# Kernel optimization log

Measured on AMD Instinct MI355X. Metric: run time of the kernel, lower is better.

## Reference

```python
import jax, jax.numpy as jnp
import numpy as np

B, S, H, NH = 1, 4096, 1024, 16
HD = H // NH  # 64


def _rope_tables(seq_len, dim):
    inv_freq = 1.0 / (10000.0 ** (np.arange(0, dim, 2, dtype=np.float32) / dim))
    t = np.arange(seq_len, dtype=np.float32)
    freqs = np.outer(t, inv_freq)                 # [S, dim/2]
    emb = np.concatenate([freqs, freqs], axis=-1)  # [S, dim]
    return jnp.asarray(np.cos(emb)), jnp.asarray(np.sin(emb))


def setup_inputs() -> dict:
    key = jax.random.key(0)
    ks = jax.random.split(key, 5)
    hidden_states = jax.random.normal(ks[0], (B, S, H), dtype=jnp.float32)
    scale = 1.0 / np.sqrt(H)
    Wq = jax.random.normal(ks[1], (H, H), dtype=jnp.float32) * scale
    Wk = jax.random.normal(ks[2], (H, H), dtype=jnp.float32) * scale
    Wv = jax.random.normal(ks[3], (H, H), dtype=jnp.float32) * scale
    Wo = jax.random.normal(ks[4], (H, H), dtype=jnp.float32) * scale
    cos, sin = _rope_tables(S, HD)
    # additive causal mask [1,1,S,S]
    causal = jnp.where(
        jnp.tril(jnp.ones((S, S), dtype=bool)), 0.0, jnp.float32(-1e9)
    )[None, None]
    return {
        "hidden_states": hidden_states,
        "cos": cos,
        "sin": sin,
        "attention_mask": causal,
        "Wq": Wq,
        "Wk": Wk,
        "Wv": Wv,
        "Wo": Wo,
    }


def _rotate_half(x):
    x1, x2 = jnp.split(x, 2, axis=-1)
    return jnp.concatenate([-x2, x1], axis=-1)


def _apply_rope(q, k, cos, sin):
    # q,k: [B,NH,S,HD]; cos/sin: [S,HD] -> broadcast [1,1,S,HD]
    cos = cos[None, None]
    sin = sin[None, None]
    q = q * cos + _rotate_half(q) * sin
    k = k * cos + _rotate_half(k) * sin
    return q, k


def reference(hidden_states, cos, sin, attention_mask, Wq, Wk, Wv, Wo):
    bsz, q_len, _ = hidden_states.shape
    q = hidden_states @ Wq.T
    k = hidden_states @ Wk.T
    v = hidden_states @ Wv.T
    # [B,S,H] -> [B,NH,S,HD]
    def split_heads(x):
        return x.reshape(bsz, q_len, NH, HD).transpose(0, 2, 1, 3)
    q, k, v = split_heads(q), split_heads(k), split_heads(v)
    q, k = _apply_rope(q, k, cos, sin)
    scores = jnp.einsum("bhqd,bhkd->bhqk", q, k) / jnp.sqrt(jnp.float32(HD))
    scores = scores + attention_mask
    attn = jax.nn.softmax(scores, axis=-1)
    out = jnp.einsum("bhqk,bhkd->bhqd", attn, v)
    out = out.transpose(0, 2, 1, 3).reshape(bsz, q_len, H)
    return out @ Wo.T
```

## Files before the change

### kernel.cpp

```cpp
#include <hip/hip_runtime.h>

#define S_LEN 4096
#define NHEADS 16
#define HD 64
#define HDIM 1024

typedef __attribute__((ext_vector_type(8))) __bf16 bf16x8;
typedef __attribute__((ext_vector_type(4))) float f32x4;
typedef __attribute__((ext_vector_type(4))) int i32x4;
typedef __attribute__((ext_vector_type(2))) int i32x2;
typedef __attribute__((ext_vector_type(4))) short s16x4;
typedef unsigned short u16;

static __device__ __forceinline__ u16 f2bu(float f) {
    unsigned u = __builtin_bit_cast(unsigned, f);
    u += 0x7FFFu + ((u >> 16) & 1u);
    return (u16)(u >> 16);
}
static __device__ __forceinline__ int pack_bf16(float lo, float hi) {
    return (int)__builtin_amdgcn_perm(__builtin_bit_cast(unsigned, hi),
                                      __builtin_bit_cast(unsigned, lo), 0x07060302u);
}
static __device__ __forceinline__ float fexp2(float x) {
    return __builtin_amdgcn_exp2f(x);
}

static __device__ __forceinline__ f32x4 mfma16(s16x4 a, s16x4 b, f32x4 c) {
#if __has_builtin(__builtin_amdgcn_mfma_f32_16x16x16bf16_1k)
    return __builtin_amdgcn_mfma_f32_16x16x16bf16_1k(a, b, c, 0, 0, 0);
#else
    asm("v_mfma_f32_16x16x16_bf16 %0, %1, %2, %0" : "+v"(c) : "v"(a), "v"(b));
    return c;
#endif
}

static __device__ __forceinline__ bf16x8 read_frag(const u16* lds, int row, int kbyte) {
    int c = kbyte ^ ((row & 7) << 4);
    return *reinterpret_cast<const bf16x8*>(reinterpret_cast<const char*>(lds) + row * 128 + c);
}
static __device__ __forceinline__ bf16x8 read_off(const u16* lds, int byteoff) {
    return *reinterpret_cast<const bf16x8*>(reinterpret_cast<const char*>(lds) + byteoff);
}
static __device__ __forceinline__ s16x4 read_off64(const u16* lds, int byteoff) {
    return *reinterpret_cast<const s16x4*>(reinterpret_cast<const char*>(lds) + byteoff);
}

static __device__ __forceinline__ void stage_gll(const u16* __restrict__ src, const u16* lds, unsigned ldsbyte) {
    __builtin_amdgcn_global_load_lds(
        (const __attribute__((address_space(1))) void*)src,
        (__attribute__((address_space(3))) void*)(reinterpret_cast<const char*>(lds) + ldsbyte),
        16, 0, 0);
}

static __device__ __forceinline__ void softmax_pack(
    const f32x4* sf, float& l_part, s16x4* pk)
{
#pragma unroll
    for (int nf = 0; nf < 4; ++nf) {
        float p0 = fexp2(sf[nf][0]);
        float p1 = fexp2(sf[nf][1]);
        float p2 = fexp2(sf[nf][2]);
        float p3 = fexp2(sf[nf][3]);
        l_part += (p0 + p1) + (p2 + p3);
        i32x2 w;
        w[0] = pack_bf16(p0, p1);
        w[1] = pack_bf16(p2, p3);
        pk[nf] = __builtin_bit_cast(s16x4, w);
    }
}

__global__ __launch_bounds__(256) void cvt_all(
    const float* __restrict__ X, const float* __restrict__ Wq, const float* __restrict__ Wk,
    const float* __restrict__ Wv, const float* __restrict__ Wo,
    u16* __restrict__ Xb, u16* __restrict__ Wqb, u16* __restrict__ Wkb,
    u16* __restrict__ Wvb, u16* __restrict__ Wob)
{
    int i = blockIdx.x * 256 + threadIdx.x;
    const float* src; u16* dst; int off;
    if (i < (1 << 20)) { src = X; dst = Xb; off = i; }
    else {
        int j = i - (1 << 20);
        int w = j >> 18; off = j & 0x3FFFF;
        src = (w == 0) ? Wq : (w == 1) ? Wk : (w == 2) ? Wv : Wo;
        dst = (w == 0) ? Wqb : (w == 1) ? Wkb : (w == 2) ? Wvb : Wob;
    }
    float4 v = reinterpret_cast<const float4*>(src)[off];
    ushort4 o;
    o.x = f2bu(v.x); o.y = f2bu(v.y); o.z = f2bu(v.z); o.w = f2bu(v.w);
    reinterpret_cast<ushort4*>(dst)[off] = o;
}

__global__ __launch_bounds__(256) void qkv_gemm(
    const u16* __restrict__ A,
    const u16* __restrict__ Wq, const u16* __restrict__ Wk, const u16* __restrict__ Wv,
    u16* __restrict__ Qb, u16* __restrict__ Kb, u16* __restrict__ VTb,
    const float* __restrict__ cosT, const float* __restrict__ sinT)
{
    __shared__ u16 At[128 * 64];
    __shared__ u16 Bt[128 * 64];
    const int z = blockIdx.z;
    const u16* W = (z == 0) ? Wq : (z == 1) ? Wk : Wv;
    const int tid = threadIdx.x;
    const int wid = tid >> 6, lane = tid & 63;
    const int wm = wid >> 1, wn = wid & 1;
    const int lj = lane >> 4, lc = lane & 15;
    const int m0 = blockIdx.x * 128, n0 = blockIdx.y * 128;

    f32x4 acc[4][4];
#pragma unroll
    for (int i = 0; i < 4; ++i)
#pragma unroll
        for (int j = 0; j < 4; ++j) acc[i][j] = 0.0f;

    for (int k0 = 0; k0 < HDIM; k0 += 64) {
        __syncthreads();
#pragma unroll
        for (int r = 0; r < 4; ++r) {
            int idx = (r << 8) + tid;
            int row = idx >> 3;
            int c = (idx & 7) << 4;
            int csw = c ^ ((row & 7) << 4);
            unsigned lb = (unsigned)(idx & ~63) << 4;
            stage_gll(A + (size_t)(m0 + row) * HDIM + k0 + (csw >> 1), At, lb);
            stage_gll(W + (size_t)(n0 + row) * HDIM + k0 + (csw >> 1), Bt, lb);
        }
        __syncthreads();
#pragma unroll
        for (int kb = 0; kb < 2; ++kb) {
            int kbyte = (kb << 6) + (lj << 4);
            bf16x8 af[4], bfr[4];
#pragma unroll
            for (int mf = 0; mf < 4; ++mf) af[mf] = read_frag(At, (wm << 6) + (mf << 4) + lc, kbyte);
#pragma unroll
            for (int nf = 0; nf < 4; ++nf) bfr[nf] = read_frag(Bt, (wn << 6) + (nf << 4) + lc, kbyte);
#pragma unroll
            for (int mf = 0; mf < 4; ++mf)
#pragma unroll
                for (int nf = 0; nf < 4; ++nf)
                    acc[mf][nf] = __builtin_amdgcn_mfma_f32_16x16x32_bf16(af[mf], bfr[nf], acc[mf][nf], 0, 0, 0);
        }
    }

    const int mrow0 = m0 + (wm << 6);
    const int ncol0 = n0 + (wn << 6);
    if (z == 2) {
#pragma unroll
        for (int mf = 0; mf < 4; ++mf)
#pragma unroll
            for (int nf = 0; nf < 4; ++nf)
#pragma unroll
                for (int j = 0; j < 4; ++j) {
                    int s = mrow0 + (mf << 4) + (lj << 2) + j;
                    int o = ncol0 + (nf << 4) + lc;
                    VTb[((size_t)(o >> 6) * HD + (o & 63)) * S_LEN + s] = f2bu(acc[mf][nf][j]);
                }
    } else {
        u16* outB = (z == 0) ? Qb : Kb;
        const float sc = (z == 0) ? 0.18033688011112042f : 1.0f;
#pragma unroll
        for (int mf = 0; mf < 4; ++mf) {
            float nv[4][4];
#pragma unroll
            for (int nf = 0; nf < 4; ++nf)
#pragma unroll
                for (int j = 0; j < 4; ++j) {
                    int s = mrow0 + (mf << 4) + (lj << 2) + j;
                    int o = ncol0 + (nf << 4) + lc;
                    int d = o & 63;
                    float x  = acc[mf][nf][j];
                    float xp = acc[mf][nf ^ 2][j];
                    float cv = cosT[(size_t)s * HD + d];
                    float sv = sinT[(size_t)s * HD + d];
                    float rot = (d < 32) ? -xp : xp;
                    nv[nf][j] = (x * cv + rot * sv) * sc;
                }
#pragma unroll
            for (int nf = 0; nf < 4; ++nf)
#pragma unroll
                for (int j = 0; j < 4; ++j) {
                    int s = mrow0 + (mf << 4) + (lj << 2) + j;
                    int o = ncol0 + (nf << 4) + lc;
                    outB[((size_t)(o >> 6) * S_LEN + s) * HD + (o & 63)] = f2bu(nv[nf][j]);
                }
        }
    }
}

__global__ __launch_bounds__(256) void wo_gemm(
    const u16* __restrict__ A, const u16* __restrict__ W, float* __restrict__ outF)
{
    __shared__ u16 At[128 * 64];
    __shared__ u16 Bt[64 * 64];
    const int tid = threadIdx.x;
    const int wid = tid >> 6, lane = tid & 63;
    const int wm = wid >> 1, wn = wid & 1;
    const int lj = lane >> 4, lc = lane & 15;
    const int m0 = blockIdx.x * 128, n0 = blockIdx.y * 64;

    f32x4 acc[4][2];
#pragma unroll
    for (int i = 0; i < 4; ++i)
#pragma unroll
        for (int j = 0; j < 2; ++j) acc[i][j] = 0.0f;

    for (int k0 = 0; k0 < HDIM; k0 += 64) {
        __syncthreads();
#pragma unroll
        for (int r = 0; r < 4; ++r) {
            int idx = (r << 8) + tid;
            int row = idx >> 3;
            int c = (idx & 7) << 4;
            int csw = c ^ ((row & 7) << 4);
            unsigned lb = (unsigned)(idx & ~63) << 4;
            stage_gll(A + (size_t)(m0 + row) * HDIM + k0 + (csw >> 1), At, lb);
            if (r < 2)
                stage_gll(W + (size_t)(n0 + row) * HDIM + k0 + (csw >> 1), Bt, lb);
        }
        __syncthreads();
#pragma unroll
        for (int kb = 0; kb < 2; ++kb) {
            int kbyte = (kb << 6) + (lj << 4);
            bf16x8 af[4], bfr[2];
#pragma unroll
            for (int mf = 0; mf < 4; ++mf) af[mf] = read_frag(At, (wm << 6) + (mf << 4) + lc, kbyte);
#pragma unroll
            for (int nf = 0; nf < 2; ++nf) bfr[nf] = read_frag(Bt, (wn << 5) + (nf << 4) + lc, kbyte);
#pragma unroll
            for (int mf = 0; mf < 4; ++mf)
#pragma unroll
                for (int nf = 0; nf < 2; ++nf)
                    acc[mf][nf] = __builtin_amdgcn_mfma_f32_16x16x32_bf16(af[mf], bfr[nf], acc[mf][nf], 0, 0, 0);
        }
    }

    const int mrow0 = m0 + (wm << 6);
    const int ncol0 = n0 + (wn << 5);
#pragma unroll
    for (int mf = 0; mf < 4; ++mf)
#pragma unroll
        for (int nf = 0; nf < 2; ++nf)
#pragma unroll
            for (int j = 0; j < 4; ++j) {
                int s = mrow0 + (mf << 4) + (lj << 2) + j;
                int o = ncol0 + (nf << 4) + lc;
                outF[(size_t)s * HDIM + o] = acc[mf][nf][j];
            }
}

__global__ __launch_bounds__(256, 2) void attn_fwd(
    const u16* __restrict__ Q, const u16* __restrict__ K,
    const u16* __restrict__ VT, u16* __restrict__ AO)
{
    __shared__ u16 Kt[2][128 * 64];
    __shared__ u16 Vt[2][2][64 * 64];

    const int tid = threadIdx.x;
    const int wid = tid >> 6, lane = tid & 63;
    const int lj = lane >> 4, lc = lane & 15;

    const int lid = blockIdx.x;
    const int x = lid & 7, g = lid >> 3;
    const int a = g >> 5, c = g & 31;
    const int qt = a ? (31 - c) : c;
    const int h = (x << 1) | a;
    const int qbase = qt * 128 + wid * 32;
    const int nsteps = 2 * qt + 2;

    const u16* Qh = Q + (size_t)h * S_LEN * HD;

    const int srow = tid >> 3;
    const int csw  = ((tid & 7) << 4) ^ ((srow & 7) << 4);
    const u16* kbase = K  + (size_t)h * S_LEN * HD + (size_t)srow * HD + (csw >> 1);
    const u16* vbase = VT + (size_t)h * HD * S_LEN + (size_t)srow * S_LEN + (csw >> 1);
    const unsigned lb = (unsigned)(tid & ~63) << 4;

#define SK(buf, hf, t) do { \
        const u16* p_ = kbase + (size_t)(t) * 64 * HD; \
        stage_gll(p_,           (const u16*)Kt[buf] + (hf) * 4096, lb); \
        stage_gll(p_ + 32 * HD, (const u16*)Kt[buf] + (hf) * 4096, lb + 4096); \
    } while (0)
#define SV(buf, hf, t) do { \
        const u16* p_ = vbase + (t) * 64; \
        stage_gll(p_,              (const u16*)Vt[buf][hf], lb); \
        stage_gll(p_ + 32 * S_LEN, (const u16*)Vt[buf][hf], lb + 4096); \
    } while (0)

    int foff[2][4];
#pragma unroll
    for (int kb = 0; kb < 2; ++kb)
#pragma unroll
        for (int nf = 0; nf < 4; ++nf) {
            int row = (nf << 4) + lc;
            foff[kb][nf] = row * 128 + (((kb << 6) + (lj << 4)) ^ ((row & 7) << 4));
        }
    int vo[4];
#pragma unroll
    for (int nf = 0; nf < 4; ++nf)
        vo[nf] = ((nf << 5) + (lj << 3)) ^ ((lc & 7) << 4);
    const int vrow = lc << 7;

    bf16x8 qB[2][2];
#pragma unroll
    for (int s = 0; s < 2; ++s)
#pragma unroll
        for (int kb = 0; kb < 2; ++kb)
            qB[s][kb] = *reinterpret_cast<const bf16x8*>(
                Qh + (size_t)(qbase + (s << 4) + lc) * HD + (kb << 5) + (lj << 3));

    f32x4 accO[2][4];
    float l0[2] = {0.0f, 0.0f};
#pragma unroll
    for (int s = 0; s < 2; ++s)
#pragma unroll
        for (int df = 0; df < 4; ++df) accO[s][df] = 0.0f;

    s16x4 pk[2][4], vf64[4][4];
    {
        i32x2 z2 = {0, 0};
#pragma unroll
        for (int nf = 0; nf < 4; ++nf) {
            pk[0][nf] = __builtin_bit_cast(s16x4, z2);
            pk[1][nf] = __builtin_bit_cast(s16x4, z2);
#pragma unroll
            for (int df = 0; df < 4; ++df) vf64[nf][df] = __builtin_bit_cast(s16x4, z2);
        }
    }

    auto compute = [&](int t, const u16* KtH, const u16* VtH) {
        bf16x8 kf[2][4];
#pragma unroll
        for (int kb = 0; kb < 2; ++kb)
#pragma unroll
            for (int nf = 0; nf < 4; ++nf)
                kf[kb][nf] = read_off(KtH, foff[kb][nf]);

        f32x4 sf[2][4];
#pragma unroll
        for (int s = 0; s < 2; ++s)
#pragma unroll
            for (int nf = 0; nf < 4; ++nf) sf[s][nf] = 0.0f;

        __builtin_amdgcn_s_setprio(1);
#pragma unroll
        for (int kb = 0; kb < 2; ++kb)
#pragma unroll
            for (int nf = 0; nf < 4; ++nf) {
                sf[0][nf] = __builtin_amdgcn_mfma_f32_16x16x32_bf16(kf[kb][nf], qB[0][kb], sf[0][nf], 0, 0, 0);
                sf[1][nf] = __builtin_amdgcn_mfma_f32_16x16x32_bf16(kf[kb][nf], qB[1][kb], sf[1][nf], 0, 0, 0);
            }
        if (t >= 1) {
#pragma unroll
            for (int nf = 0; nf < 4; ++nf)
#pragma unroll
                for (int df = 0; df < 4; ++df) {
                    accO[0][df] = mfma16(pk[0][nf], vf64[nf][df], accO[0][df]);
                    accO[1][df] = mfma16(pk[1][nf], vf64[nf][df], accO[1][df]);
                }
        }
        __builtin_amdgcn_s_setprio(0);

#pragma unroll
        for (int nf = 0; nf < 4; ++nf)
#pragma unroll
            for (int df = 0; df < 4; ++df)
                vf64[nf][df] = read_off64(VtH, (df << 11) + vrow + vo[nf]);

        if (t >= 2 * qt) {
            int kv0 = t << 6;
#pragma unroll
            for (int s = 0; s < 2; ++s) {
                int qg = qbase + (s << 4) + lc;
#pragma unroll
                for (int nf = 0; nf < 4; ++nf)
#pragma unroll
                    for (int jj = 0; jj < 4; ++jj) {
                        int kvg = kv0 + (nf << 4) + (lj << 2) + jj;
                        if (kvg > qg) sf[s][nf][jj] = -1e30f;
                    }
            }
        }

        softmax_pack(sf[0], l0[0], pk[0]);
        softmax_pack(sf[1], l0[1], pk[1]);
    };

    SK(0, 0, 0); SV(0, 0, 0);
    SK(0, 1, 1); SV(0, 1, 1);
    __syncthreads();

    const int nmac = nsteps >> 1;
    int cur = 0;
    for (int m = 0; m < nmac; ++m) {
        const int t2 = 2 * m + 2, t3 = 2 * m + 3;
        if (t2 < nsteps) { SK(cur ^ 1, 0, t2); SV(cur ^ 1, 0, t2); }
        if (t3 < nsteps) { SK(cur ^ 1, 1, t3); SV(cur ^ 1, 1, t3); }

        compute(2 * m, (const u16*)Kt[cur], (const u16*)Vt[cur][0]);
        compute(2 * m + 1, (const u16*)Kt[cur] + 4096, (const u16*)Vt[cur][1]);

        __syncthreads();
        cur ^= 1;
    }

#pragma unroll
    for (int nf = 0; nf < 4; ++nf)
#pragma unroll
        for (int df = 0; df < 4; ++df) {
            accO[0][df] = mfma16(pk[0][nf], vf64[nf][df], accO[0][df]);
            accO[1][df] = mfma16(pk[1][nf], vf64[nf][df], accO[1][df]);
        }

#pragma unroll
    for (int s = 0; s < 2; ++s) {
        float lp = l0[s];
        lp += __shfl_xor(lp, 16); lp += __shfl_xor(lp, 32);
        float lr[4];
#pragma unroll
        for (int jj = 0; jj < 4; ++jj) lr[jj] = __shfl(lp, (lj << 2) + jj);
#pragma unroll
        for (int df = 0; df < 4; ++df)
#pragma unroll
            for (int jj = 0; jj < 4; ++jj) {
                int sq = qbase + (s << 4) + (lj << 2) + jj;
                int d = (df << 4) + lc;
                AO[(size_t)sq * HDIM + h * HD + d] = f2bu(accO[s][df][jj] / lr[jj]);
            }
    }
#undef SK
#undef SV
}

extern "C" void kernel_launch(void* const* d_in, const int* in_sizes, int n_in,
                              void* d_out, int out_size, void* d_ws, size_t ws_size,
                              hipStream_t stream) {
    const float* hidden = (const float*)d_in[0];
    const float* cosT   = (const float*)d_in[1];
    const float* sinT   = (const float*)d_in[2];
    const float* Wq = (const float*)d_in[4];
    const float* Wk = (const float*)d_in[5];
    const float* Wv = (const float*)d_in[6];
    const float* Wo = (const float*)d_in[7];
    float* out = (float*)d_out;

    char* ws = (char*)d_ws;
    u16* Xb  = (u16*)(ws);
    u16* Wqb = (u16*)(ws + (size_t)( 8 << 20));
    u16* Wkb = (u16*)(ws + (size_t)(10 << 20));
    u16* Wvb = (u16*)(ws + (size_t)(12 << 20));
    u16* Wob = (u16*)(ws + (size_t)(14 << 20));
    u16* Qb  = (u16*)(ws + (size_t)(16 << 20));
    u16* Kb  = (u16*)(ws + (size_t)(24 << 20));
    u16* VTb = (u16*)(ws + (size_t)(32 << 20));
    u16* AOb = (u16*)(ws + (size_t)(40 << 20));

    cvt_all<<<8192, 256, 0, stream>>>(hidden, Wq, Wk, Wv, Wo, Xb, Wqb, Wkb, Wvb, Wob);

    qkv_gemm<<<dim3(S_LEN / 128, HDIM / 128, 3), 256, 0, stream>>>(
        Xb, Wqb, Wkb, Wvb, Qb, Kb, VTb, cosT, sinT);

    attn_fwd<<<dim3(512), 256, 0, stream>>>(Qb, Kb, VTb, AOb);

    wo_gemm<<<dim3(S_LEN / 128, HDIM / 64), 256, 0, stream>>>(AOb, Wob, out);
}
```

Baseline: 157.1 us.

## Double-buffer LDS staging in QKV and output-projection GEMMs

Both projection GEMMs now keep two LDS buffers and issue the global-to-LDS load for the next K tile before computing on the current one. One barrier per iteration replaces the previous two, so load latency can overlap the MFMA work. Launch bounds are raised to request 2 and 3 blocks per CU to keep occupancy despite the doubled shared memory. The risks are register pressure from the tighter bounds and a possible wait on outstanding async loads before the barrier.

```diff
diff --git a/kernel.cpp b/kernel.cpp
--- a/kernel.cpp
+++ b/kernel.cpp
@@ -90,14 +90,14 @@
     reinterpret_cast<ushort4*>(dst)[off] = o;
 }
 
-__global__ __launch_bounds__(256) void qkv_gemm(
+__global__ __launch_bounds__(256, 2) void qkv_gemm(
     const u16* __restrict__ A,
     const u16* __restrict__ Wq, const u16* __restrict__ Wk, const u16* __restrict__ Wv,
     u16* __restrict__ Qb, u16* __restrict__ Kb, u16* __restrict__ VTb,
     const float* __restrict__ cosT, const float* __restrict__ sinT)
 {
-    __shared__ u16 At[128 * 64];
-    __shared__ u16 Bt[128 * 64];
+    __shared__ u16 At[2][128 * 64];
+    __shared__ u16 Bt[2][128 * 64];
     const int z = blockIdx.z;
     const u16* W = (z == 0) ? Wq : (z == 1) ? Wk : Wv;
     const int tid = threadIdx.x;
@@ -106,39 +106,45 @@
     const int lj = lane >> 4, lc = lane & 15;
     const int m0 = blockIdx.x * 128, n0 = blockIdx.y * 128;
 
+#define STG(buf, k0) do { \
+        _Pragma("unroll") \
+        for (int r = 0; r < 4; ++r) { \
+            int idx = (r << 8) + tid; \
+            int row = idx >> 3; \
+            int csw2 = (((idx & 7) << 4) ^ ((row & 7) << 4)) >> 1; \
+            unsigned lbb = (unsigned)(idx & ~63) << 4; \
+            stage_gll(A + (size_t)(m0 + row) * HDIM + (k0) + csw2, At[buf], lbb); \
+            stage_gll(W + (size_t)(n0 + row) * HDIM + (k0) + csw2, Bt[buf], lbb); \
+        } } while (0)
+
     f32x4 acc[4][4];
 #pragma unroll
     for (int i = 0; i < 4; ++i)
 #pragma unroll
         for (int j = 0; j < 4; ++j) acc[i][j] = 0.0f;
 
-    for (int k0 = 0; k0 < HDIM; k0 += 64) {
-        __syncthreads();
-#pragma unroll
-        for (int r = 0; r < 4; ++r) {
-            int idx = (r << 8) + tid;
-            int row = idx >> 3;
-            int c = (idx & 7) << 4;
-            int csw = c ^ ((row & 7) << 4);
-            unsigned lb = (unsigned)(idx & ~63) << 4;
-            stage_gll(A + (size_t)(m0 + row) * HDIM + k0 + (csw >> 1), At, lb);
-            stage_gll(W + (size_t)(n0 + row) * HDIM + k0 + (csw >> 1), Bt, lb);
-        }
-        __syncthreads();
+    STG(0, 0);
+    __syncthreads();
+
+    int cur = 0;
+    for (int kk = 0; kk < HDIM / 64; ++kk) {
+        if (kk + 1 < HDIM / 64) STG(cur ^ 1, (kk + 1) * 64);
 #pragma unroll
         for (int kb = 0; kb < 2; ++kb) {
             int kbyte = (kb << 6) + (lj << 4);
             bf16x8 af[4], bfr[4];
 #pragma unroll
-            for (int mf = 0; mf < 4; ++mf) af[mf] = read_frag(At, (wm << 6) + (mf << 4) + lc, kbyte);
-#pragma unroll
-            for (int nf = 0; nf < 4; ++nf) bfr[nf] = read_frag(Bt, (wn << 6) + (nf << 4) + lc, kbyte);
+            for (int mf = 0; mf < 4; ++mf) af[mf] = read_frag(At[cur], (wm << 6) + (mf << 4) + lc, kbyte);
+#pragma unroll
+            for (int nf = 0; nf < 4; ++nf) bfr[nf] = read_frag(Bt[cur], (wn << 6) + (nf << 4) + lc, kbyte);
 #pragma unroll
             for (int mf = 0; mf < 4; ++mf)
 #pragma unroll
                 for (int nf = 0; nf < 4; ++nf)
                     acc[mf][nf] = __builtin_amdgcn_mfma_f32_16x16x32_bf16(af[mf], bfr[nf], acc[mf][nf], 0, 0, 0);
         }
+        __syncthreads();
+        cur ^= 1;
     }
 
     const int mrow0 = m0 + (wm << 6);
@@ -184,53 +190,60 @@
                 }
         }
     }
-}
-
-__global__ __launch_bounds__(256) void wo_gemm(
+#undef STG
+}
+
+__global__ __launch_bounds__(256, 3) void wo_gemm(
     const u16* __restrict__ A, const u16* __restrict__ W, float* __restrict__ outF)
 {
-    __shared__ u16 At[128 * 64];
-    __shared__ u16 Bt[64 * 64];
+    __shared__ u16 At[2][128 * 64];
+    __shared__ u16 Bt[2][64 * 64];
     const int tid = threadIdx.x;
     const int wid = tid >> 6, lane = tid & 63;
     const int wm = wid >> 1, wn = wid & 1;
     const int lj = lane >> 4, lc = lane & 15;
     const int m0 = blockIdx.x * 128, n0 = blockIdx.y * 64;
 
+#define STG(buf, k0) do { \
+        _Pragma("unroll") \
+        for (int r = 0; r < 4; ++r) { \
+            int idx = (r << 8) + tid; \
+            int row = idx >> 3; \
+            int csw2 = (((idx & 7) << 4) ^ ((row & 7) << 4)) >> 1; \
+            unsigned lbb = (unsigned)(idx & ~63) << 4; \
+            stage_gll(A + (size_t)(m0 + row) * HDIM + (k0) + csw2, At[buf], lbb); \
+            if (r < 2) \
+                stage_gll(W + (size_t)(n0 + row) * HDIM + (k0) + csw2, Bt[buf], lbb); \
+        } } while (0)
+
     f32x4 acc[4][2];
 #pragma unroll
     for (int i = 0; i < 4; ++i)
 #pragma unroll
         for (int j = 0; j < 2; ++j) acc[i][j] = 0.0f;
 
-    for (int k0 = 0; k0 < HDIM; k0 += 64) {
-        __syncthreads();
-#pragma unroll
-        for (int r = 0; r < 4; ++r) {
-            int idx = (r << 8) + tid;
-            int row = idx >> 3;
-            int c = (idx & 7) << 4;
-            int csw = c ^ ((row & 7) << 4);
-            unsigned lb = (unsigned)(idx & ~63) << 4;
-            stage_gll(A + (size_t)(m0 + row) * HDIM + k0 + (csw >> 1), At, lb);
-            if (r < 2)
-                stage_gll(W + (size_t)(n0 + row) * HDIM + k0 + (csw >> 1), Bt, lb);
-        }
-        __syncthreads();
+    STG(0, 0);
+    __syncthreads();
+
+    int cur = 0;
+    for (int kk = 0; kk < HDIM / 64; ++kk) {
+        if (kk + 1 < HDIM / 64) STG(cur ^ 1, (kk + 1) * 64);
 #pragma unroll
         for (int kb = 0; kb < 2; ++kb) {
             int kbyte = (kb << 6) + (lj << 4);
             bf16x8 af[4], bfr[2];
 #pragma unroll
-            for (int mf = 0; mf < 4; ++mf) af[mf] = read_frag(At, (wm << 6) + (mf << 4) + lc, kbyte);
-#pragma unroll
-            for (int nf = 0; nf < 2; ++nf) bfr[nf] = read_frag(Bt, (wn << 5) + (nf << 4) + lc, kbyte);
+            for (int mf = 0; mf < 4; ++mf) af[mf] = read_frag(At[cur], (wm << 6) + (mf << 4) + lc, kbyte);
+#pragma unroll
+            for (int nf = 0; nf < 2; ++nf) bfr[nf] = read_frag(Bt[cur], (wn << 5) + (nf << 4) + lc, kbyte);
 #pragma unroll
             for (int mf = 0; mf < 4; ++mf)
 #pragma unroll
                 for (int nf = 0; nf < 2; ++nf)
                     acc[mf][nf] = __builtin_amdgcn_mfma_f32_16x16x32_bf16(af[mf], bfr[nf], acc[mf][nf], 0, 0, 0);
         }
+        __syncthreads();
+        cur ^= 1;
     }
 
     const int mrow0 = m0 + (wm << 6);
@@ -245,6 +258,7 @@
                 int o = ncol0 + (nf << 4) + lc;
                 outF[(size_t)s * HDIM + o] = acc[mf][nf][j];
             }
+#undef STG
 }
 
 __global__ __launch_bounds__(256, 2) void attn_fwd(
```

New measurement: 134.2 us. 1.17x faster.
